# Performance work log

Hardware: AMD Instinct MI355X
Metric: run time of the kernel (lower is better)

## Reference

```python
import jax, jax.numpy as jnp
import numpy as np
import math

EMBED = 1024
HEADS = 16
HEAD_DIM = EMBED // HEADS  # 64
BSZ = 32
TGT = 512   # == src_len, required by the bmm-over-sequence structure
SRC = 512   # == BSZ*HEADS, required by the need_weights view


def _xavier(k, shape):
    fan_out, fan_in = shape
    limit = math.sqrt(6.0 / (fan_in + fan_out))
    return jax.random.uniform(k, shape, jnp.float32, -limit, limit)


def setup_inputs() -> dict:
    key = jax.random.key(0)
    ks = jax.random.split(key, 8)
    d = EMBED
    return {
        # query given as [bsz, tgt_len, d]; the module transposes it internally
        "query": jax.random.normal(ks[0], (BSZ, TGT, d), jnp.float32),
        "key": jax.random.normal(ks[1], (SRC, BSZ, d), jnp.float32),
        "value": jax.random.normal(ks[2], (SRC, BSZ, d), jnp.float32),
        "Wq": _xavier(ks[3], (d, d)), "bq": jnp.zeros((d,), jnp.float32),
        "Wk": _xavier(ks[4], (d, d)), "bk": jnp.zeros((d,), jnp.float32),
        "Wv": _xavier(ks[5], (d, d)), "bv": jnp.zeros((d,), jnp.float32),
        "Wo": _xavier(ks[6], (d, d)), "bo": jnp.zeros((d,), jnp.float32),
    }


def reference(query, key, value, Wq, bq, Wk, bk, Wv, bv, Wo, bo):
    H, hd = HEADS, HEAD_DIM
    # module transposes [bsz, tgt_len, d] -> [tgt_len, bsz, d]
    query = jnp.transpose(query, (1, 0, 2))
    T, B, D = query.shape
    S = key.shape[0]  # == T and == B*H by construction
    # projections (nn.Linear: x @ W.T + b)
    q = (query @ Wq.T + bq).reshape(T, B * H, hd)
    k = (key @ Wk.T + bk).reshape(S, B * H, hd)
    v = (value @ Wv.T + bv).reshape(S, B * H, hd)
    # torch.bmm with the SEQUENCE dim as the bmm batch dim (faithful to source):
    # scores: [T, BH, BH]
    scores = jnp.einsum('tbd,tcd->tbc', q, k) / jnp.sqrt(jnp.asarray(hd, q.dtype))
    attn = jax.nn.softmax(scores, axis=-1)  # dropout p=0.0, eval mode
    out = jnp.einsum('tbc,tcd->tbd', attn, v)  # [T, BH, hd]
    out = out.reshape(T, B, D) @ Wo.T + bo     # [T, B, D]
    # need_weights=True branch: view [T,H,B,S], permute(2,1,0,3), mean over heads
    w = attn.reshape(T, H, B, S).transpose(2, 1, 0, 3).mean(axis=1)  # [B, T, S]
    return out, w
```

## Files before the change

kernel.cpp:

```cpp
#include <hip/hip_runtime.h>
#include <hip/hip_bf16.h>
#include <stdint.h>


typedef __attribute__((ext_vector_type(8))) short bf16x8;
typedef __attribute__((ext_vector_type(4))) float f32x4;
typedef unsigned short u16;
typedef unsigned int u32;

typedef __attribute__((address_space(1))) const unsigned int as1_u32;
typedef __attribute__((address_space(3))) unsigned int as3_u32;

__device__ __forceinline__ void glds16(const void* g, void* l) {
    __builtin_amdgcn_global_load_lds((as1_u32*)g, (as3_u32*)l, 16, 0, 0);
}

__device__ __forceinline__ u16 f2bf(float f) {
    u32 u = __builtin_bit_cast(u32, f);
    u32 r = (u + 0x7FFFu + ((u >> 16) & 1u)) >> 16;
    return (u16)r;
}

__device__ __forceinline__ bf16x8 pk8(float4 a, float4 b) {
    union { bf16x8 v; u16 h[8]; } o;
    o.h[0] = f2bf(a.x); o.h[1] = f2bf(a.y); o.h[2] = f2bf(a.z); o.h[3] = f2bf(a.w);
    o.h[4] = f2bf(b.x); o.h[5] = f2bf(b.y); o.h[6] = f2bf(b.z); o.h[7] = f2bf(b.w);
    return o.v;
}

template <int CTRL>
__device__ __forceinline__ float dpp_add(float x) {
    int xi = __builtin_bit_cast(int, x);
    int yi = __builtin_amdgcn_update_dpp(0, xi, CTRL, 0xF, 0xF, true);
    return x + __builtin_bit_cast(float, yi);
}
__device__ __forceinline__ float red16(float v) {
    v = dpp_add<0xB1>(v);
    v = dpp_add<0x4E>(v);
    v = dpp_add<0x141>(v);
    v = dpp_add<0x140>(v);
    return v;
}

__global__ void convw_kernel(const float4* __restrict__ Wq, const float4* __restrict__ Wk,
                             const float4* __restrict__ Wv, const float4* __restrict__ Wo,
                             uint2* __restrict__ wqb, uint2* __restrict__ wkb,
                             uint2* __restrict__ wvb, uint2* __restrict__ wob) {
    const int NT = gridDim.x * blockDim.x;
    for (int i = blockIdx.x * blockDim.x + threadIdx.x; i < 1048576; i += NT) {
        int wsel = i >> 18, di = i & 262143;
        const float4* s = wsel == 0 ? Wq : wsel == 1 ? Wk : wsel == 2 ? Wv : Wo;
        uint2* d = wsel == 0 ? wqb : wsel == 1 ? wkb : wsel == 2 ? wvb : wob;
        float4 v = s[di];
        uint2 r;
        r.x = (u32)f2bf(v.x) | ((u32)f2bf(v.y) << 16);
        r.y = (u32)f2bf(v.z) | ((u32)f2bf(v.w) << 16);
        d[di] = r;
    }
}

__global__ __launch_bounds__(256, 2)
void gemm3_kernel(const float* __restrict__ Aq, const float* __restrict__ Ak,
                  const float* __restrict__ Av,
                  const u16* __restrict__ Bq, const u16* __restrict__ Bk,
                  const u16* __restrict__ Bv,
                  const float* __restrict__ bq, const float* __restrict__ bk,
                  const float* __restrict__ bv,
                  u16* __restrict__ Cq, u16* __restrict__ Ck, u16* __restrict__ Cv) {
    __shared__ __align__(16) u16 As[8192];
    __shared__ __align__(16) u16 Bs[2][8192];
    const int z = blockIdx.z;
    const float* A = z == 0 ? Aq : z == 1 ? Ak : Av;
    const u16* B = z == 0 ? Bq : z == 1 ? Bk : Bv;
    const float* bias = z == 0 ? bq : z == 1 ? bk : bv;
    u16* C = z == 0 ? Cq : z == 1 ? Ck : Cv;
    const bool qremap = (z == 0);
    const int tid = threadIdx.x;
    const int id = blockIdx.x;
    const int xcd = id & 7, j = id >> 3;
    const int ny = j & 7, band = xcd * 16 + (j >> 3);
    const long N0 = (long)ny * 128;
    const long M0 = (long)band * 128;
    const int lane = tid & 63, wv = tid >> 6;
    const int l15 = lane & 15, g = lane >> 4;
    const int wm = (wv >> 1) * 64, wn = (wv & 1) * 64;

    bf16x8 stA[4];
    auto loadA = [&](int kt) {
#pragma unroll
        for (int i2 = 0; i2 < 4; ++i2) {
            int q = tid + 256 * i2; int r = q >> 3, c16 = q & 7;
            long m = M0 + r;
            long row = qremap ? ((m & 31) * 512 + (m >> 5)) : m;
            const float* ap = A + row * 1024 + kt * 64 + c16 * 8;
            float4 f0 = *(const float4*)ap;
            float4 f1 = *(const float4*)(ap + 4);
            stA[i2] = pk8(f0, f1);
        }
    };
    auto writeA = [&]() {
#pragma unroll
        for (int i2 = 0; i2 < 4; ++i2) {
            int q = tid + 256 * i2; int r = q >> 3, c16 = q & 7;
            int d = r * 128 + ((c16 * 16) ^ ((r & 7) << 4));
            *(bf16x8*)((char*)As + d) = stA[i2];
        }
    };
    auto gldsB = [&](int kt, int buf) {
#pragma unroll
        for (int i2 = 0; i2 < 4; ++i2) {
            int q = tid + 256 * i2; int r = q >> 3, c16 = q & 7;
            int c16s = c16 ^ (r & 7);
            char* ldsbase = (char*)Bs[buf] + (i2 * 256 + wv * 64) * 16;
            glds16(B + (N0 + r) * 1024 + kt * 64 + c16s * 8, ldsbase);
        }
    };
    gldsB(0, 0);
    loadA(0);
    writeA();
    __syncthreads();
    f32x4 acc[4][4] = {};
    const int swz = (l15 & 7) << 4;
    for (int kt = 0; kt < 16; ++kt) {
        if (kt < 15) { gldsB(kt + 1, (kt + 1) & 1); loadA(kt + 1); }
        const char* Bcur = (const char*)Bs[kt & 1];
#pragma unroll
        for (int kk = 0; kk < 2; ++kk) {
            bf16x8 av[4], bvv[4];
#pragma unroll
            for (int mt = 0; mt < 4; ++mt) {
                int row = wm + mt * 16 + l15;
                av[mt] = *(const bf16x8*)((const char*)As + row * 128 + ((kk * 64 + g * 16) ^ swz));
            }
#pragma unroll
            for (int nt = 0; nt < 4; ++nt) {
                int row = wn + nt * 16 + l15;
                bvv[nt] = *(const bf16x8*)(Bcur + row * 128 + ((kk * 64 + g * 16) ^ swz));
            }
#pragma unroll
            for (int mt = 0; mt < 4; ++mt)
#pragma unroll
                for (int nt = 0; nt < 4; ++nt)
                    acc[mt][nt] = __builtin_amdgcn_mfma_f32_16x16x32_bf16(av[mt], bvv[nt], acc[mt][nt], 0, 0, 0);
        }
        __syncthreads();
        if (kt < 15) { writeA(); __syncthreads(); }
    }
    float bsv[4];
#pragma unroll
    for (int nt = 0; nt < 4; ++nt) bsv[nt] = bias[N0 + wn + nt * 16 + l15];
#pragma unroll
    for (int mt = 0; mt < 4; ++mt)
#pragma unroll
        for (int nt = 0; nt < 4; ++nt)
#pragma unroll
            for (int r = 0; r < 4; ++r) {
                long m = M0 + wm + mt * 16 + g * 4 + r;
                long n = N0 + wn + nt * 16 + l15;
                C[m * 1024 + n] = f2bf(acc[mt][nt][r] + bsv[nt]);
            }
}

__global__ __launch_bounds__(256, 2)
void gemm_out_kernel(const u16* __restrict__ A, const u16* __restrict__ B,
                     const float* __restrict__ bias, float* __restrict__ C) {
    __shared__ __align__(16) u16 As[2][8192];
    __shared__ __align__(16) u16 Bs[2][8192];
    const int tid = threadIdx.x;
    const int id = blockIdx.x;
    const int xcd = id & 7, j = id >> 3;
    const int ny = j & 7, band = xcd * 16 + (j >> 3);
    const long N0 = (long)ny * 128;
    const long M0 = (long)band * 128;
    const int lane = tid & 63, wv = tid >> 6;
    const int l15 = lane & 15, g = lane >> 4;
    const int wm = (wv >> 1) * 64, wn = (wv & 1) * 64;

    auto gldsAB = [&](int kt, int buf) {
#pragma unroll
        for (int i2 = 0; i2 < 4; ++i2) {
            int q = tid + 256 * i2; int r = q >> 3, c16 = q & 7;
            int c16s = c16 ^ (r & 7);
            char* lbA = (char*)As[buf] + (i2 * 256 + wv * 64) * 16;
            char* lbB = (char*)Bs[buf] + (i2 * 256 + wv * 64) * 16;
            glds16(A + (M0 + r) * 1024 + kt * 64 + c16s * 8, lbA);
            glds16(B + (N0 + r) * 1024 + kt * 64 + c16s * 8, lbB);
        }
    };
    gldsAB(0, 0);
    __syncthreads();
    f32x4 acc[4][4] = {};
    const int swz = (l15 & 7) << 4;
    for (int kt = 0; kt < 16; ++kt) {
        if (kt < 15) gldsAB(kt + 1, (kt + 1) & 1);
        const char* Acur = (const char*)As[kt & 1];
        const char* Bcur = (const char*)Bs[kt & 1];
#pragma unroll
        for (int kk = 0; kk < 2; ++kk) {
            bf16x8 av[4], bvv[4];
#pragma unroll
            for (int mt = 0; mt < 4; ++mt) {
                int row = wm + mt * 16 + l15;
                av[mt] = *(const bf16x8*)(Acur + row * 128 + ((kk * 64 + g * 16) ^ swz));
            }
#pragma unroll
            for (int nt = 0; nt < 4; ++nt) {
                int row = wn + nt * 16 + l15;
                bvv[nt] = *(const bf16x8*)(Bcur + row * 128 + ((kk * 64 + g * 16) ^ swz));
            }
#pragma unroll
            for (int mt = 0; mt < 4; ++mt)
#pragma unroll
                for (int nt = 0; nt < 4; ++nt)
                    acc[mt][nt] = __builtin_amdgcn_mfma_f32_16x16x32_bf16(av[mt], bvv[nt], acc[mt][nt], 0, 0, 0);
        }
        __syncthreads();
    }
    float bsv[4];
#pragma unroll
    for (int nt = 0; nt < 4; ++nt) bsv[nt] = bias[N0 + wn + nt * 16 + l15];
#pragma unroll
    for (int mt = 0; mt < 4; ++mt)
#pragma unroll
        for (int nt = 0; nt < 4; ++nt)
#pragma unroll
            for (int r = 0; r < 4; ++r) {
                long m = M0 + wm + mt * 16 + g * 4 + r;
                long n = N0 + wn + nt * 16 + l15;
                C[m * 1024 + n] = acc[mt][nt][r] + bsv[nt];
            }
}

__global__ __launch_bounds__(512, 2)
void attn_kernel(const u16* __restrict__ Q, const u16* __restrict__ K,
                 const u16* __restrict__ V, u16* __restrict__ ctx,
                 float* __restrict__ wout) {
    __shared__ __align__(16) char smem[32768];
    const int bid = blockIdx.x;
    const int wk_ = (bid & 7) * 256 + (bid >> 3);
    const int t = wk_ >> 2, it = wk_ & 3;
    const int tid = threadIdx.x, lane = tid & 63, wv = tid >> 6;
    const int l15 = lane & 15, g = lane >> 4;
    const int swk = (l15 & 7) << 4;
    const int bb = it * 8 + wv;
    const float ksc = 0.18033688011112042f;

    const u16* Kt = K + (size_t)t * 32768;
    const u16* Vt = V + (size_t)t * 32768;

    auto stageK = [&](int q, int slot) {
#pragma unroll
        for (int hh = 0; hh < 2; ++hh) {
            int idx = hh * 512 + tid;
            int sl = idx >> 3, c16 = idx & 7;
            int csw = c16 ^ (sl & 7);
            glds16(Kt + (size_t)(q * 128 + sl) * 64 + csw * 8,
                   smem + slot * 16384 + hh * 8192 + wv * 1024);
        }
    };
    bf16x8 vreg[2];
    auto loadV = [&](int q) {
#pragma unroll
        for (int hh = 0; hh < 2; ++hh) {
            int u = hh * 512 + tid;
            int sl = u >> 3, ec = u & 7;
            vreg[hh] = *(const bf16x8*)(Vt + (size_t)(q * 128 + sl) * 64 + ec * 8);
        }
    };
    auto writeV = [&](int slot) {
        char* base = smem + slot * 16384;
#pragma unroll
        for (int hh = 0; hh < 2; ++hh) {
            int u = hh * 512 + tid;
            int sl = u >> 3, ec = u & 7;
#pragma unroll
            for (int jj = 0; jj < 8; ++jj) {
                int swv = (jj ^ (ec & 3)) << 4;
                *(u16*)(base + (ec * 8 + jj) * 256 + ((sl * 2) ^ swv)) = (u16)vreg[hh][jj];
            }
        }
    };
    f32x4 pv[4];
    auto pvQuarter = [&](const char* vb, bf16x8 p0, bf16x8 p1, bf16x8 p2, bf16x8 p3) {
        bf16x8 pq[4] = {p0, p1, p2, p3};
        __builtin_amdgcn_s_setprio(1);
#pragma unroll
        for (int m = 0; m < 4; ++m) {
#pragma unroll
            for (int nt = 0; nt < 4; ++nt) {
                int e = nt * 16 + l15;
                int esw = ((e & 7) ^ ((e >> 3) & 3)) << 4;
                const char* vrow = vb + e * 256;
                union { bf16x8 v; uint2 uu[2]; } bv;
                bv.uu[0] = *(const uint2*)(vrow + ((m * 64 + 8 * g) ^ esw));
                bv.uu[1] = *(const uint2*)(vrow + ((m * 64 + 32 + 8 * g) ^ esw));
                pv[nt] = __builtin_amdgcn_mfma_f32_16x16x32_bf16(pq[m], bv.v, pv[nt], 0, 0, 0);
            }
        }
        __builtin_amdgcn_s_setprio(0);
    };

    const int c = 32 * l15 + bb;
    const u16* qrow = Q + ((size_t)t * 512 + c) * 64;
    bf16x8 qb0 = *(const bf16x8*)(qrow + g * 8);
    bf16x8 qb1 = *(const bf16x8*)(qrow + 32 + g * 8);

    stageK(0, 0);
    __syncthreads();
    float sum = 0.f;
    bf16x8 pP[16];
#pragma unroll
    for (int q = 0; q < 4; ++q) {
        if (q < 3) stageK(q + 1, (q + 1) & 1);
        else loadV(0);
        const char* kb = smem + (q & 1) * 16384;
        __builtin_amdgcn_s_setprio(1);
#pragma unroll
        for (int m = 0; m < 4; ++m) {
            union { bf16x8 v; u32 u[4]; } pa;
#pragma unroll
            for (int h2 = 0; h2 < 2; ++h2) {
                int lsl = 2 * m + h2;
                const char* rowp = kb + (lsl * 16 + l15) * 128;
                bf16x8 a0 = *(const bf16x8*)(rowp + ((g * 16) ^ swk));
                bf16x8 a1 = *(const bf16x8*)(rowp + ((64 + g * 16) ^ swk));
                f32x4 zz = {0.f, 0.f, 0.f, 0.f};
                zz = __builtin_amdgcn_mfma_f32_16x16x32_bf16(a0, qb0, zz, 0, 0, 0);
                zz = __builtin_amdgcn_mfma_f32_16x16x32_bf16(a1, qb1, zz, 0, 0, 0);
                float e0 = exp2f(zz[0] * ksc), e1 = exp2f(zz[1] * ksc);
                float e2 = exp2f(zz[2] * ksc), e3 = exp2f(zz[3] * ksc);
                sum += (e0 + e1) + (e2 + e3);
                pa.u[2 * h2]     = (u32)f2bf(e0) | ((u32)f2bf(e1) << 16);
                pa.u[2 * h2 + 1] = (u32)f2bf(e2) | ((u32)f2bf(e3) << 16);
            }
            pP[q * 4 + m] = pa.v;
        }
        __builtin_amdgcn_s_setprio(0);
        __syncthreads();
    }
    sum += __shfl_xor(sum, 16);
    sum += __shfl_xor(sum, 32);
    const float inv = 1.f / sum;

    writeV(0);
    loadV(1);

    {
        const float inv16 = inv * 0.0625f;
        float4 wreg0 = {0.f, 0.f, 0.f, 0.f}, wreg1 = {0.f, 0.f, 0.f, 0.f};
#pragma unroll
        for (int st = 0; st < 32; ++st) {
            union { bf16x8 v; u32 u[4]; } pu; pu.v = pP[st >> 1];
            u32 ua = pu.u[(st & 1) * 2], ub = pu.u[(st & 1) * 2 + 1];
            float v0 = __builtin_bit_cast(float, (ua & 0xFFFFu) << 16) * inv16;
            float v1 = __builtin_bit_cast(float, ua & 0xFFFF0000u) * inv16;
            float v2 = __builtin_bit_cast(float, (ub & 0xFFFFu) << 16) * inv16;
            float v3 = __builtin_bit_cast(float, ub & 0xFFFF0000u) * inv16;
            v0 = red16(v0); v1 = red16(v1); v2 = red16(v2); v3 = red16(v3);
            if ((st >> 1) == l15) {
                if (st & 1) wreg1 = (float4){v0, v1, v2, v3};
                else        wreg0 = (float4){v0, v1, v2, v3};
            }
        }
        float* wrow = wout + ((size_t)(bb * 512 + t)) * 512 + 32 * l15 + 4 * g;
        *(float4*)(wrow) = wreg0;
        *(float4*)(wrow + 16) = wreg1;
    }
    __syncthreads();

#pragma unroll
    for (int nt = 0; nt < 4; ++nt) pv[nt] = (f32x4){0.f, 0.f, 0.f, 0.f};
    writeV(1);
    pvQuarter(smem, pP[0], pP[1], pP[2], pP[3]);
    loadV(2);
    __syncthreads();
    writeV(0);
    pvQuarter(smem + 16384, pP[4], pP[5], pP[6], pP[7]);
    loadV(3);
    __syncthreads();
    writeV(1);
    pvQuarter(smem, pP[8], pP[9], pP[10], pP[11]);
    __syncthreads();
    pvQuarter(smem + 16384, pP[12], pP[13], pP[14], pP[15]);

    float invv[4];
#pragma unroll
    for (int r = 0; r < 4; ++r) invv[r] = __shfl(inv, g * 4 + r);
#pragma unroll
    for (int nt = 0; nt < 4; ++nt)
#pragma unroll
        for (int r = 0; r < 4; ++r)
            ctx[((size_t)t * 512 + 32 * (g * 4 + r) + bb) * 64 + nt * 16 + l15] =
                f2bf(pv[nt][r] * invv[r]);
}

extern "C" void kernel_launch(void* const* d_in, const int* in_sizes, int n_in,
                              void* d_out, int out_size, void* d_ws, size_t ws_size,
                              hipStream_t stream) {
    const float* query = (const float*)d_in[0];
    const float* key   = (const float*)d_in[1];
    const float* value = (const float*)d_in[2];
    const float* Wq = (const float*)d_in[3];  const float* bq = (const float*)d_in[4];
    const float* Wk = (const float*)d_in[5];  const float* bk = (const float*)d_in[6];
    const float* Wv = (const float*)d_in[7];  const float* bv = (const float*)d_in[8];
    const float* Wo = (const float*)d_in[9];  const float* bo = (const float*)d_in[10];

    char* ws = (char*)d_ws;
    u16* wqb  = (u16*)(ws + 0);
    u16* wkb  = (u16*)(ws + 2097152);
    u16* wvb  = (u16*)(ws + 4194304);
    u16* wob  = (u16*)(ws + 6291456);
    u16* q_ws = (u16*)(ws + 8388608);
    u16* k_ws = (u16*)(ws + 41943040);
    u16* v_ws = (u16*)(ws + 75497472);

    float* out  = (float*)d_out;
    float* wout = out + 16777216;

    convw_kernel<<<1024, 256, 0, stream>>>(
        (const float4*)Wq, (const float4*)Wk, (const float4*)Wv, (const float4*)Wo,
        (uint2*)wqb, (uint2*)wkb, (uint2*)wvb, (uint2*)wob);

    dim3 gg3(1024, 1, 3);
    gemm3_kernel<<<gg3, 256, 0, stream>>>(query, key, value, wqb, wkb, wvb,
                                          bq, bk, bv, q_ws, k_ws, v_ws);

    attn_kernel<<<2048, 512, 0, stream>>>(q_ws, k_ws, v_ws, q_ws, wout);

    gemm_out_kernel<<<1024, 256, 0, stream>>>(q_ws, wob, bo, out);
}
```

Measured before the change: 378.9 us.

## Load GEMM A operands straight from global memory and pre-transpose query to bf16

The A operand of the projection GEMMs is no longer staged in LDS. Each wave loads its A fragments directly from global memory, converting from fp32 when needed, and only B is double-buffered through LDS. The query transpose and bf16 conversion move into the weight-conversion kernel, which writes a contiguous bf16 buffer. The fused three-way GEMM becomes three separate launches of one templated kernel, and the output GEMM uses the same kernel. This removes LDS writes and barriers for A, at the cost of uncoalesced, unshared global A loads that are repeated across the two N-waves, an extra pass over query, and more launches.

```diff
diff --git a/kernel.cpp b/kernel.cpp
--- a/kernel.cpp
+++ b/kernel.cpp
@@ -42,16 +42,27 @@
     return v;
 }
 
-__global__ void convw_kernel(const float4* __restrict__ Wq, const float4* __restrict__ Wk,
+__global__ void convw_kernel(const float4* __restrict__ query,
+                             const float4* __restrict__ Wq, const float4* __restrict__ Wk,
                              const float4* __restrict__ Wv, const float4* __restrict__ Wo,
+                             uint2* __restrict__ qx,
                              uint2* __restrict__ wqb, uint2* __restrict__ wkb,
                              uint2* __restrict__ wvb, uint2* __restrict__ wob) {
     const int NT = gridDim.x * blockDim.x;
-    for (int i = blockIdx.x * blockDim.x + threadIdx.x; i < 1048576; i += NT) {
-        int wsel = i >> 18, di = i & 262143;
-        const float4* s = wsel == 0 ? Wq : wsel == 1 ? Wk : wsel == 2 ? Wv : Wo;
-        uint2* d = wsel == 0 ? wqb : wsel == 1 ? wkb : wsel == 2 ? wvb : wob;
-        float4 v = s[di];
+    for (int i = blockIdx.x * blockDim.x + threadIdx.x; i < 5242880; i += NT) {
+        float4 v; uint2* d; int di;
+        if (i < 4194304) {
+            int m = i >> 8, c4 = i & 255;
+            int t = m >> 5, b = m & 31;
+            v = query[(b * 512 + t) * 256 + c4];
+            d = qx; di = i;
+        } else {
+            int jj = i - 4194304;
+            int wsel = jj >> 18; di = jj & 262143;
+            const float4* s = wsel == 0 ? Wq : wsel == 1 ? Wk : wsel == 2 ? Wv : Wo;
+            d = wsel == 0 ? wqb : wsel == 1 ? wkb : wsel == 2 ? wvb : wob;
+            v = s[di];
+        }
         uint2 r;
         r.x = (u32)f2bf(v.x) | ((u32)f2bf(v.y) << 16);
         r.y = (u32)f2bf(v.z) | ((u32)f2bf(v.w) << 16);
@@ -59,112 +70,11 @@
     }
 }
 
+template <int F32OUT>
 __global__ __launch_bounds__(256, 2)
-void gemm3_kernel(const float* __restrict__ Aq, const float* __restrict__ Ak,
-                  const float* __restrict__ Av,
-                  const u16* __restrict__ Bq, const u16* __restrict__ Bk,
-                  const u16* __restrict__ Bv,
-                  const float* __restrict__ bq, const float* __restrict__ bk,
-                  const float* __restrict__ bv,
-                  u16* __restrict__ Cq, u16* __restrict__ Ck, u16* __restrict__ Cv) {
-    __shared__ __align__(16) u16 As[8192];
-    __shared__ __align__(16) u16 Bs[2][8192];
-    const int z = blockIdx.z;
-    const float* A = z == 0 ? Aq : z == 1 ? Ak : Av;
-    const u16* B = z == 0 ? Bq : z == 1 ? Bk : Bv;
-    const float* bias = z == 0 ? bq : z == 1 ? bk : bv;
-    u16* C = z == 0 ? Cq : z == 1 ? Ck : Cv;
-    const bool qremap = (z == 0);
-    const int tid = threadIdx.x;
-    const int id = blockIdx.x;
-    const int xcd = id & 7, j = id >> 3;
-    const int ny = j & 7, band = xcd * 16 + (j >> 3);
-    const long N0 = (long)ny * 128;
-    const long M0 = (long)band * 128;
-    const int lane = tid & 63, wv = tid >> 6;
-    const int l15 = lane & 15, g = lane >> 4;
-    const int wm = (wv >> 1) * 64, wn = (wv & 1) * 64;
-
-    bf16x8 stA[4];
-    auto loadA = [&](int kt) {
-#pragma unroll
-        for (int i2 = 0; i2 < 4; ++i2) {
-            int q = tid + 256 * i2; int r = q >> 3, c16 = q & 7;
-            long m = M0 + r;
-            long row = qremap ? ((m & 31) * 512 + (m >> 5)) : m;
-            const float* ap = A + row * 1024 + kt * 64 + c16 * 8;
-            float4 f0 = *(const float4*)ap;
-            float4 f1 = *(const float4*)(ap + 4);
-            stA[i2] = pk8(f0, f1);
-        }
-    };
-    auto writeA = [&]() {
-#pragma unroll
-        for (int i2 = 0; i2 < 4; ++i2) {
-            int q = tid + 256 * i2; int r = q >> 3, c16 = q & 7;
-            int d = r * 128 + ((c16 * 16) ^ ((r & 7) << 4));
-            *(bf16x8*)((char*)As + d) = stA[i2];
-        }
-    };
-    auto gldsB = [&](int kt, int buf) {
-#pragma unroll
-        for (int i2 = 0; i2 < 4; ++i2) {
-            int q = tid + 256 * i2; int r = q >> 3, c16 = q & 7;
-            int c16s = c16 ^ (r & 7);
-            char* ldsbase = (char*)Bs[buf] + (i2 * 256 + wv * 64) * 16;
-            glds16(B + (N0 + r) * 1024 + kt * 64 + c16s * 8, ldsbase);
-        }
-    };
-    gldsB(0, 0);
-    loadA(0);
-    writeA();
-    __syncthreads();
-    f32x4 acc[4][4] = {};
-    const int swz = (l15 & 7) << 4;
-    for (int kt = 0; kt < 16; ++kt) {
-        if (kt < 15) { gldsB(kt + 1, (kt + 1) & 1); loadA(kt + 1); }
-        const char* Bcur = (const char*)Bs[kt & 1];
-#pragma unroll
-        for (int kk = 0; kk < 2; ++kk) {
-            bf16x8 av[4], bvv[4];
-#pragma unroll
-            for (int mt = 0; mt < 4; ++mt) {
-                int row = wm + mt * 16 + l15;
-                av[mt] = *(const bf16x8*)((const char*)As + row * 128 + ((kk * 64 + g * 16) ^ swz));
-            }
-#pragma unroll
-            for (int nt = 0; nt < 4; ++nt) {
-                int row = wn + nt * 16 + l15;
-                bvv[nt] = *(const bf16x8*)(Bcur + row * 128 + ((kk * 64 + g * 16) ^ swz));
-            }
-#pragma unroll
-            for (int mt = 0; mt < 4; ++mt)
-#pragma unroll
-                for (int nt = 0; nt < 4; ++nt)
-                    acc[mt][nt] = __builtin_amdgcn_mfma_f32_16x16x32_bf16(av[mt], bvv[nt], acc[mt][nt], 0, 0, 0);
-        }
-        __syncthreads();
-        if (kt < 15) { writeA(); __syncthreads(); }
-    }
-    float bsv[4];
-#pragma unroll
-    for (int nt = 0; nt < 4; ++nt) bsv[nt] = bias[N0 + wn + nt * 16 + l15];
-#pragma unroll
-    for (int mt = 0; mt < 4; ++mt)
-#pragma unroll
-        for (int nt = 0; nt < 4; ++nt)
-#pragma unroll
-            for (int r = 0; r < 4; ++r) {
-                long m = M0 + wm + mt * 16 + g * 4 + r;
-                long n = N0 + wn + nt * 16 + l15;
-                C[m * 1024 + n] = f2bf(acc[mt][nt][r] + bsv[nt]);
-            }
-}
-
-__global__ __launch_bounds__(256, 2)
-void gemm_out_kernel(const u16* __restrict__ A, const u16* __restrict__ B,
-                     const float* __restrict__ bias, float* __restrict__ C) {
-    __shared__ __align__(16) u16 As[2][8192];
+void gemm_direct(const void* __restrict__ Ap, int af32,
+                 const u16* __restrict__ Bw,
+                 const float* __restrict__ bias, void* __restrict__ Cp) {
     __shared__ __align__(16) u16 Bs[2][8192];
     const int tid = threadIdx.x;
     const int id = blockIdx.x;
@@ -176,33 +86,39 @@
     const int l15 = lane & 15, g = lane >> 4;
     const int wm = (wv >> 1) * 64, wn = (wv & 1) * 64;
 
-    auto gldsAB = [&](int kt, int buf) {
+    auto gldsB = [&](int kt, int buf) {
 #pragma unroll
         for (int i2 = 0; i2 < 4; ++i2) {
             int q = tid + 256 * i2; int r = q >> 3, c16 = q & 7;
             int c16s = c16 ^ (r & 7);
-            char* lbA = (char*)As[buf] + (i2 * 256 + wv * 64) * 16;
-            char* lbB = (char*)Bs[buf] + (i2 * 256 + wv * 64) * 16;
-            glds16(A + (M0 + r) * 1024 + kt * 64 + c16s * 8, lbA);
-            glds16(B + (N0 + r) * 1024 + kt * 64 + c16s * 8, lbB);
-        }
-    };
-    gldsAB(0, 0);
+            char* ldsbase = (char*)Bs[buf] + (i2 * 256 + wv * 64) * 16;
+            glds16(Bw + (N0 + r) * 1024 + kt * 64 + c16s * 8, ldsbase);
+        }
+    };
+    auto loadAfrag = [&](int kt, int kk, int mt) -> bf16x8 {
+        long row = M0 + wm + mt * 16 + l15;
+        long ko = kt * 64 + kk * 32 + g * 8;
+        if (af32) {
+            const float* ap = (const float*)Ap + row * 1024 + ko;
+            float4 f0 = *(const float4*)ap;
+            float4 f1 = *(const float4*)(ap + 4);
+            return pk8(f0, f1);
+        }
+        return *(const bf16x8*)((const u16*)Ap + row * 1024 + ko);
+    };
+
+    gldsB(0, 0);
     __syncthreads();
     f32x4 acc[4][4] = {};
     const int swz = (l15 & 7) << 4;
     for (int kt = 0; kt < 16; ++kt) {
-        if (kt < 15) gldsAB(kt + 1, (kt + 1) & 1);
-        const char* Acur = (const char*)As[kt & 1];
+        if (kt < 15) gldsB(kt + 1, (kt + 1) & 1);
         const char* Bcur = (const char*)Bs[kt & 1];
 #pragma unroll
         for (int kk = 0; kk < 2; ++kk) {
             bf16x8 av[4], bvv[4];
 #pragma unroll
-            for (int mt = 0; mt < 4; ++mt) {
-                int row = wm + mt * 16 + l15;
-                av[mt] = *(const bf16x8*)(Acur + row * 128 + ((kk * 64 + g * 16) ^ swz));
-            }
+            for (int mt = 0; mt < 4; ++mt) av[mt] = loadAfrag(kt, kk, mt);
 #pragma unroll
             for (int nt = 0; nt < 4; ++nt) {
                 int row = wn + nt * 16 + l15;
@@ -227,7 +143,9 @@
             for (int r = 0; r < 4; ++r) {
                 long m = M0 + wm + mt * 16 + g * 4 + r;
                 long n = N0 + wn + nt * 16 + l15;
-                C[m * 1024 + n] = acc[mt][nt][r] + bsv[nt];
+                float v = acc[mt][nt][r] + bsv[nt];
+                if (F32OUT) ((float*)Cp)[m * 1024 + n] = v;
+                else        ((u16*)Cp)[m * 1024 + n] = f2bf(v);
             }
 }
 
@@ -413,19 +331,21 @@
     u16* q_ws = (u16*)(ws + 8388608);
     u16* k_ws = (u16*)(ws + 41943040);
     u16* v_ws = (u16*)(ws + 75497472);
+    u16* qx   = (u16*)(ws + 109051904);
 
     float* out  = (float*)d_out;
     float* wout = out + 16777216;
 
-    convw_kernel<<<1024, 256, 0, stream>>>(
+    convw_kernel<<<2048, 256, 0, stream>>>(
+        (const float4*)query,
         (const float4*)Wq, (const float4*)Wk, (const float4*)Wv, (const float4*)Wo,
-        (uint2*)wqb, (uint2*)wkb, (uint2*)wvb, (uint2*)wob);
-
-    dim3 gg3(1024, 1, 3);
-    gemm3_kernel<<<gg3, 256, 0, stream>>>(query, key, value, wqb, wkb, wvb,
-                                          bq, bk, bv, q_ws, k_ws, v_ws);
+        (uint2*)qx, (uint2*)wqb, (uint2*)wkb, (uint2*)wvb, (uint2*)wob);
+
+    gemm_direct<0><<<1024, 256, 0, stream>>>(qx,    0, wqb, bq, q_ws);
+    gemm_direct<0><<<1024, 256, 0, stream>>>(key,   1, wkb, bk, k_ws);
+    gemm_direct<0><<<1024, 256, 0, stream>>>(value, 1, wvb, bv, v_ws);
 
     attn_kernel<<<2048, 512, 0, stream>>>(q_ws, k_ws, v_ws, q_ws, wout);
 
-    gemm_out_kernel<<<1024, 256, 0, stream>>>(q_ws, wob, bo, out);
-}
+    gemm_direct<1><<<1024, 256, 0, stream>>>(q_ws, 0, wob, bo, out);
+}
```

Measured after the change: 558.8 us. +47.5%, slower.

## Pre-transpose query to bf16 and double-buffer A tile in QKV GEMM

Applied to the files above, without the earlier changes.

The weight-conversion kernel now also converts the query tensor to bf16 in the transposed [T,B] row order, so the Q projection GEMM reads contiguous bf16 rows instead of strided fp32 rows through a remap. The GEMM's A tile in shared memory is double-buffered, so the next tile is written after the MFMA loop and one barrier per k-step is removed. This adds an extra pass over the query tensor (read fp32, write bf16) and doubles A's LDS footprint, which could affect occupancy.

```diff
diff --git a/kernel.cpp b/kernel.cpp
--- a/kernel.cpp
+++ b/kernel.cpp
@@ -42,16 +42,27 @@
     return v;
 }
 
-__global__ void convw_kernel(const float4* __restrict__ Wq, const float4* __restrict__ Wk,
+__global__ void convw_kernel(const float4* __restrict__ query,
+                             const float4* __restrict__ Wq, const float4* __restrict__ Wk,
                              const float4* __restrict__ Wv, const float4* __restrict__ Wo,
+                             uint2* __restrict__ qx,
                              uint2* __restrict__ wqb, uint2* __restrict__ wkb,
                              uint2* __restrict__ wvb, uint2* __restrict__ wob) {
     const int NT = gridDim.x * blockDim.x;
-    for (int i = blockIdx.x * blockDim.x + threadIdx.x; i < 1048576; i += NT) {
-        int wsel = i >> 18, di = i & 262143;
-        const float4* s = wsel == 0 ? Wq : wsel == 1 ? Wk : wsel == 2 ? Wv : Wo;
-        uint2* d = wsel == 0 ? wqb : wsel == 1 ? wkb : wsel == 2 ? wvb : wob;
-        float4 v = s[di];
+    for (int i = blockIdx.x * blockDim.x + threadIdx.x; i < 5242880; i += NT) {
+        float4 v; uint2* d; int di;
+        if (i < 4194304) {
+            int m = i >> 8, c4 = i & 255;
+            int t = m >> 5, b = m & 31;
+            v = query[(b * 512 + t) * 256 + c4];
+            d = qx; di = i;
+        } else {
+            int jj = i - 4194304;
+            int wsel = jj >> 18; di = jj & 262143;
+            const float4* s = wsel == 0 ? Wq : wsel == 1 ? Wk : wsel == 2 ? Wv : Wo;
+            d = wsel == 0 ? wqb : wsel == 1 ? wkb : wsel == 2 ? wvb : wob;
+            v = s[di];
+        }
         uint2 r;
         r.x = (u32)f2bf(v.x) | ((u32)f2bf(v.y) << 16);
         r.y = (u32)f2bf(v.z) | ((u32)f2bf(v.w) << 16);
@@ -60,21 +71,19 @@
 }
 
 __global__ __launch_bounds__(256, 2)
-void gemm3_kernel(const float* __restrict__ Aq, const float* __restrict__ Ak,
+void gemm3_kernel(const u16* __restrict__ Aq, const float* __restrict__ Ak,
                   const float* __restrict__ Av,
                   const u16* __restrict__ Bq, const u16* __restrict__ Bk,
                   const u16* __restrict__ Bv,
                   const float* __restrict__ bq, const float* __restrict__ bk,
                   const float* __restrict__ bv,
                   u16* __restrict__ Cq, u16* __restrict__ Ck, u16* __restrict__ Cv) {
-    __shared__ __align__(16) u16 As[8192];
+    __shared__ __align__(16) u16 As[2][8192];
     __shared__ __align__(16) u16 Bs[2][8192];
     const int z = blockIdx.z;
-    const float* A = z == 0 ? Aq : z == 1 ? Ak : Av;
     const u16* B = z == 0 ? Bq : z == 1 ? Bk : Bv;
     const float* bias = z == 0 ? bq : z == 1 ? bk : bv;
     u16* C = z == 0 ? Cq : z == 1 ? Ck : Cv;
-    const bool qremap = (z == 0);
     const int tid = threadIdx.x;
     const int id = blockIdx.x;
     const int xcd = id & 7, j = id >> 3;
@@ -91,19 +100,23 @@
         for (int i2 = 0; i2 < 4; ++i2) {
             int q = tid + 256 * i2; int r = q >> 3, c16 = q & 7;
             long m = M0 + r;
-            long row = qremap ? ((m & 31) * 512 + (m >> 5)) : m;
-            const float* ap = A + row * 1024 + kt * 64 + c16 * 8;
-            float4 f0 = *(const float4*)ap;
-            float4 f1 = *(const float4*)(ap + 4);
-            stA[i2] = pk8(f0, f1);
-        }
-    };
-    auto writeA = [&]() {
+            if (z == 0) {
+                stA[i2] = *(const bf16x8*)(Aq + m * 1024 + kt * 64 + c16 * 8);
+            } else {
+                const float* A = (z == 1) ? Ak : Av;
+                const float* ap = A + m * 1024 + kt * 64 + c16 * 8;
+                float4 f0 = *(const float4*)ap;
+                float4 f1 = *(const float4*)(ap + 4);
+                stA[i2] = pk8(f0, f1);
+            }
+        }
+    };
+    auto writeA = [&](int buf) {
 #pragma unroll
         for (int i2 = 0; i2 < 4; ++i2) {
             int q = tid + 256 * i2; int r = q >> 3, c16 = q & 7;
             int d = r * 128 + ((c16 * 16) ^ ((r & 7) << 4));
-            *(bf16x8*)((char*)As + d) = stA[i2];
+            *(bf16x8*)((char*)As[buf] + d) = stA[i2];
         }
     };
     auto gldsB = [&](int kt, int buf) {
@@ -115,22 +128,24 @@
             glds16(B + (N0 + r) * 1024 + kt * 64 + c16s * 8, ldsbase);
         }
     };
+    loadA(0);
     gldsB(0, 0);
-    loadA(0);
-    writeA();
+    writeA(0);
     __syncthreads();
     f32x4 acc[4][4] = {};
     const int swz = (l15 & 7) << 4;
     for (int kt = 0; kt < 16; ++kt) {
-        if (kt < 15) { gldsB(kt + 1, (kt + 1) & 1); loadA(kt + 1); }
-        const char* Bcur = (const char*)Bs[kt & 1];
+        const int cb = kt & 1, nb = cb ^ 1;
+        if (kt < 15) { loadA(kt + 1); gldsB(kt + 1, nb); }
+        const char* Acur = (const char*)As[cb];
+        const char* Bcur = (const char*)Bs[cb];
 #pragma unroll
         for (int kk = 0; kk < 2; ++kk) {
             bf16x8 av[4], bvv[4];
 #pragma unroll
             for (int mt = 0; mt < 4; ++mt) {
                 int row = wm + mt * 16 + l15;
-                av[mt] = *(const bf16x8*)((const char*)As + row * 128 + ((kk * 64 + g * 16) ^ swz));
+                av[mt] = *(const bf16x8*)(Acur + row * 128 + ((kk * 64 + g * 16) ^ swz));
             }
 #pragma unroll
             for (int nt = 0; nt < 4; ++nt) {
@@ -143,8 +158,8 @@
                 for (int nt = 0; nt < 4; ++nt)
                     acc[mt][nt] = __builtin_amdgcn_mfma_f32_16x16x32_bf16(av[mt], bvv[nt], acc[mt][nt], 0, 0, 0);
         }
+        if (kt < 15) writeA(nb);
         __syncthreads();
-        if (kt < 15) { writeA(); __syncthreads(); }
     }
     float bsv[4];
 #pragma unroll
@@ -413,16 +428,18 @@
     u16* q_ws = (u16*)(ws + 8388608);
     u16* k_ws = (u16*)(ws + 41943040);
     u16* v_ws = (u16*)(ws + 75497472);
+    u16* qx   = (u16*)(ws + 109051904);
 
     float* out  = (float*)d_out;
     float* wout = out + 16777216;
 
-    convw_kernel<<<1024, 256, 0, stream>>>(
+    convw_kernel<<<2048, 256, 0, stream>>>(
+        (const float4*)query,
         (const float4*)Wq, (const float4*)Wk, (const float4*)Wv, (const float4*)Wo,
-        (uint2*)wqb, (uint2*)wkb, (uint2*)wvb, (uint2*)wob);
+        (uint2*)qx, (uint2*)wqb, (uint2*)wkb, (uint2*)wvb, (uint2*)wob);
 
     dim3 gg3(1024, 1, 3);
-    gemm3_kernel<<<gg3, 256, 0, stream>>>(query, key, value, wqb, wkb, wvb,
+    gemm3_kernel<<<gg3, 256, 0, stream>>>(qx, key, value, wqb, wkb, wvb,
                                           bq, bk, bv, q_ws, k_ws, v_ws);
 
     attn_kernel<<<2048, 512, 0, stream>>>(q_ws, k_ws, v_ws, q_ws, wout);
```

Measured after the change: 474.7 us. 25.3% more time.
